# Optimization experiments

Measured on AMD Instinct MI355X. Metric: run time of the kernel, lower is better.

## Reference

```python
import jax, jax.numpy as jnp
import numpy as np
from jax import lax

EPS = 1e-5
QUANT_BITS = 16  # Conv2dShift default input fixed-point bits


def round_fixed(x, quant_bits=QUANT_BITS):
    # fixed-point rounding of activations with straight-through estimator
    scale = 2.0 ** (quant_bits - 1)
    xq = jnp.round(x * scale) / scale
    return x + lax.stop_gradient(xq - x)


def shift_conv3x3(x, w_shift, stride=1):
    # w_shift already holds sign * 2^shift power-of-two weights (see setup)
    x = round_fixed(x)
    return lax.conv_general_dilated(
        x, w_shift, window_strides=(stride, stride), padding=[(1, 1), (1, 1)],
        dimension_numbers=("NCHW", "OIHW", "NCHW"))


def adder_conv3x3(x, w):
    # AdderNet: out[n,co,h,w] = -sum_{ci,kh,kw} |patch - w[co,ci,kh,kw]|
    Co = w.shape[0]
    # patches: [N, C*3*3, H, W], feature ordering (c, kh, kw) matches w.reshape
    p = lax.conv_general_dilated_patches(
        x, filter_shape=(3, 3), window_strides=(1, 1), padding=[(1, 1), (1, 1)])
    wf = w.reshape(Co, -1)

    def per_out_channel(wc):  # wc: [C*9]
        return -jnp.sum(jnp.abs(p - wc[None, :, None, None]), axis=1)  # [N,H,W]

    out = lax.map(per_out_channel, wf)  # [Co, N, H, W] (sequential: bounds memory)
    return jnp.transpose(out, (1, 0, 2, 3))


def batch_norm(x, gamma, beta):
    # training-mode BN (batch statistics), matching nn.BatchNorm2d default forward
    m = jnp.mean(x, axis=(0, 2, 3), keepdims=True)
    v = jnp.var(x, axis=(0, 2, 3), keepdims=True)
    xn = (x - m) * lax.rsqrt(v + EPS)
    return xn * gamma.reshape(1, -1, 1, 1) + beta.reshape(1, -1, 1, 1)


def _quantize_shift_weights(w, weight_bits=5):
    # DeepShift PS: weight -> sign * 2^round(log2|w|), shift clipped
    sign = jnp.where(w >= 0, 1.0, -1.0)
    shift = jnp.round(jnp.log2(jnp.abs(w) + 1e-12))
    shift = jnp.clip(shift, -(2.0 ** (weight_bits - 1) - 1.0), 0.0)
    return sign * jnp.exp2(shift)


def setup_inputs() -> dict:
    key = jax.random.key(0)
    ks = jax.random.split(key, 9)
    N, C, H, W = 64, 128, 32, 32
    planes = 128
    fan = 1.0 / np.sqrt(C * 9)
    x = jax.random.normal(ks[0], (N, C, H, W), dtype=jnp.float32)
    w_shift1 = _quantize_shift_weights(
        jax.random.normal(ks[1], (planes, C, 3, 3), dtype=jnp.float32) * fan)
    w_add1 = jax.random.normal(ks[2], (planes, planes, 3, 3), dtype=jnp.float32) * fan
    w_shift2 = _quantize_shift_weights(
        jax.random.normal(ks[3], (planes, planes, 3, 3), dtype=jnp.float32) * fan)
    w_add2 = jax.random.normal(ks[4], (planes, planes, 3, 3), dtype=jnp.float32) * fan
    gamma1 = jnp.ones((planes,), jnp.float32)
    beta1 = jnp.zeros((planes,), jnp.float32)
    gamma2 = jnp.ones((planes,), jnp.float32)
    beta2 = jnp.zeros((planes,), jnp.float32)
    return {"x": x, "w_shift1": w_shift1, "w_add1": w_add1, "gamma1": gamma1,
            "beta1": beta1, "w_shift2": w_shift2, "w_add2": w_add2,
            "gamma2": gamma2, "beta2": beta2}


def reference(x, w_shift1, w_add1, gamma1, beta1, w_shift2, w_add2, gamma2, beta2):
    residual = x
    out = shift_conv3x3(x, w_shift1, stride=1)
    out = adder_conv3x3(out, w_add1)
    out = jax.nn.relu(batch_norm(out, gamma1, beta1))
    out = shift_conv3x3(out, w_shift2, stride=1)
    out = adder_conv3x3(out, w_add2)
    out = batch_norm(out, gamma2, beta2)
    out = jax.nn.relu(out + residual)
    return out
```

## Files before the change

### kernel.cpp

```cpp
#include <hip/hip_runtime.h>


#define NB   64
#define CIN  128
#define HW   32
#define COUT 128
constexpr int PLANE    = HW * HW;
constexpr int NPAIR    = CIN / 2;
constexpr int CI_CHUNK = 4;
constexpr int CO_CHUNK = 8;
constexpr int LPLANE   = 34 * 32;
constexpr int LDS_TOT  = 2 * CI_CHUNK * LPLANE;
constexpr int A_CI     = 2;
constexpr int A_CO     = 4;
constexpr int A_LDS    = 2 * A_CI * LPLANE;
constexpr float FSCALE    = 32768.0f;
constexpr float INV_SCALE = 1.0f / 32768.0f;
constexpr float QS     = 2048.0f;
constexpr float QB     = 32768.5f;
constexpr float INV_QS = 1.0f / 2048.0f;
constexpr unsigned PZ  = 0x80008000u;

constexpr int G_ROWB   = 32 * 8 * 16;
constexpr int G_CIQB   = 34 * G_ROWB;
constexpr int G_NB     = 4 * G_CIQB;

typedef _Float16 f16x8 __attribute__((ext_vector_type(8)));
typedef float    f32x4 __attribute__((ext_vector_type(4)));

#define GLOBAL_AS __attribute__((address_space(1)))
#define LDS_AS    __attribute__((address_space(3)))

__device__ __forceinline__ void gload_lds16(const void* g, void* l) {
    __builtin_amdgcn_global_load_lds((const GLOBAL_AS void*)g, (LDS_AS void*)l,
                                     16, 0, 0);
}
__device__ __forceinline__ float dpp_prev(float x) {
    return __int_as_float(__builtin_amdgcn_update_dpp(
        0, __float_as_int(x), 0x111, 0xF, 0xF, true));
}
__device__ __forceinline__ float dpp_next(float x) {
    return __int_as_float(__builtin_amdgcn_update_dpp(
        0, __float_as_int(x), 0x101, 0xF, 0xF, true));
}
__device__ __forceinline__ unsigned dpp_prev_u(unsigned x) {
    return (unsigned)__builtin_amdgcn_update_dpp(0, (int)x, 0x111, 0xF, 0xF, true);
}
__device__ __forceinline__ unsigned dpp_next_u(unsigned x) {
    return (unsigned)__builtin_amdgcn_update_dpp(0, (int)x, 0x101, 0xF, 0xF, true);
}
__device__ __forceinline__ uint4 dpp4_shr(uint4 v) {
    uint4 r;
    r.x = dpp_prev_u(v.x); r.y = dpp_prev_u(v.y);
    r.z = dpp_prev_u(v.z); r.w = dpp_prev_u(v.w);
    return r;
}
__device__ __forceinline__ uint4 dpp4_shl(uint4 v) {
    uint4 r;
    r.x = dpp_next_u(v.x); r.y = dpp_next_u(v.y);
    r.z = dpp_next_u(v.z); r.w = dpp_next_u(v.w);
    return r;
}
__device__ __forceinline__ void stage_plane4(const void* src, void* dst, int lane) {
#pragma unroll
    for (int i = 0; i < 4; ++i)
        gload_lds16((const char*)src + i * 1024 + lane * 16,
                    (char*)dst + 128 + i * 1024);
}
__device__ __forceinline__ unsigned q16(float a) {
    float t = fmaf(a, QS, QB);
    t = fminf(fmaxf(t, 0.0f), 65535.0f);
    return (unsigned)t;
}
__device__ __forceinline__ unsigned packhl(float v) {
    _Float16 h = (_Float16)v;
    _Float16 l = (_Float16)(v - (float)h);
    unsigned uh = (unsigned)__builtin_bit_cast(unsigned short, h);
    unsigned ul = (unsigned)__builtin_bit_cast(unsigned short, l);
    return uh | (ul << 16);
}

template <int WITH_BN>
__global__ __launch_bounds__(256) void transform_split(
    const float* __restrict__ in, const float* __restrict__ scale,
    const float* __restrict__ bias, uint4* __restrict__ G)
{
    __shared__ float sT[32 * 132];
    const int tid = threadIdx.x;
    const int b   = blockIdx.x;
    const int n   = b >> 5;
    const int ciq = (b >> 3) & 3;
    const int rq  = b & 7;

#pragma unroll
    for (int it = 0; it < 4; ++it) {
        int flat = it * 256 + tid;
        int ci_rel = flat >> 5;
        int px4 = (flat & 31) * 4;
        const float* ap = in + ((size_t)(n * CIN + ciq * 32 + ci_rel)) * PLANE
                             + rq * 128 + px4;
        float4 v = *reinterpret_cast<const float4*>(ap);
        if (WITH_BN) {
            float sc = scale[ciq * 32 + ci_rel], bs = bias[ciq * 32 + ci_rel];
            v.x = fmaxf(fmaf(v.x, sc, bs), 0.0f);
            v.y = fmaxf(fmaf(v.y, sc, bs), 0.0f);
            v.z = fmaxf(fmaf(v.z, sc, bs), 0.0f);
            v.w = fmaxf(fmaf(v.w, sc, bs), 0.0f);
        }
        v.x = rintf(v.x * FSCALE) * INV_SCALE;
        v.y = rintf(v.y * FSCALE) * INV_SCALE;
        v.z = rintf(v.z * FSCALE) * INV_SCALE;
        v.w = rintf(v.w * FSCALE) * INV_SCALE;
        *reinterpret_cast<float4*>(&sT[ci_rel * 132 + px4]) = v;
    }
    __syncthreads();

    uint4* Gp = G + ((size_t)n * G_NB + ciq * G_CIQB) / 16;
#pragma unroll
    for (int it = 0; it < 4; ++it) {
        int f = it * 256 + tid;
        int row_loc = f >> 8;
        int rem = f & 255;
        int w  = rem >> 3;
        int sg = rem & 7;
        int g  = sg ^ (w & 7);
        uint4 u;
        unsigned* up = &u.x;
#pragma unroll
        for (int j = 0; j < 4; ++j)
            up[j] = packhl(sT[(g * 4 + j) * 132 + row_loc * 32 + w]);
        int gr = rq * 4 + row_loc + 1;
        Gp[(gr * 32 + w) * 8 + sg] = u;
    }
    if (rq == 0) Gp[tid] = make_uint4(0, 0, 0, 0);
    if (rq == 7) Gp[33 * 256 + tid] = make_uint4(0, 0, 0, 0);
}

__global__ __launch_bounds__(256) void wf_prep(
    const float* __restrict__ w1, const float* __restrict__ w2,
    unsigned* __restrict__ WF)
{
    int i = blockIdx.x * 256 + threadIdx.x;
    int layer = i >= 147456;
    int idx = i - layer * 147456;
    int j2  = idx & 3;
    int l   = (idx >> 2) & 63;
    int cot = (idx >> 8) & 7;
    int kch = (idx >> 11) & 1;
    int ciq = (idx >> 12) & 3;
    int tap = idx >> 14;
    int ci  = ciq * 32 + kch * 16 + (l >> 4) * 4 + j2;
    int co  = cot * 16 + (l & 15);
    const float* w = layer ? w2 : w1;
    float v = w[((size_t)co * CIN + ci) * 9 + tap];
    unsigned h = (unsigned)__builtin_bit_cast(unsigned short, (_Float16)v);
    WF[i] = h | (h << 16);
}

__global__ __launch_bounds__(256, 2) void conv_mfma(
    const uint4* __restrict__ G, const uint4* __restrict__ WF,
    unsigned* __restrict__ P)
{
    __shared__ uint4 sA[1536];
    const int tid  = threadIdx.x;
    const int lane = tid & 63;
    const int wid  = tid >> 6;
    const int b    = (blockIdx.x & 7) * 64 + (blockIdx.x >> 3);
    const int n    = b >> 3;
    const int q4   = b & 7;
    const int glo16 = (lane >> 4) * 16;

    f32x4 acc[8][2];
#pragma unroll
    for (int i = 0; i < 8; ++i)
#pragma unroll
        for (int j = 0; j < 2; ++j) acc[i][j] = (f32x4){0.f, 0.f, 0.f, 0.f};

    for (int ciq = 0; ciq < 4; ++ciq) {
        if (ciq) __syncthreads();
        const char* src = (const char*)G + (size_t)n * G_NB + ciq * G_CIQB
                        + (size_t)q4 * 4 * G_ROWB;
#pragma unroll
        for (int i = 0; i < 6; ++i) {
            int off = i * 4096 + wid * 1024;
            gload_lds16(src + off + lane * 16, (char*)sA + off);
        }
        __syncthreads();

#pragma unroll
        for (int kch = 0; kch < 2; ++kch) {
            uint4 Brow[2][3];
            int pwh[2];
#pragma unroll
            for (int half = 0; half < 2; ++half) {
                pwh[half] = half * 16 + (lane & 15);
                int cb = ((kch * 64) | glo16) ^ ((pwh[half] & 7) * 16);
#pragma unroll
                for (int rr = 0; rr < 3; ++rr)
                    Brow[half][rr] = *reinterpret_cast<const uint4*>(
                        (const char*)sA + (wid + rr) * 4096 + pwh[half] * 128 + cb);
            }
#pragma unroll
            for (int dh = 0; dh < 3; ++dh)
#pragma unroll
            for (int dw = 0; dw < 3; ++dw) {
                const uint4* wfp = WF
                    + ((size_t)(((dh * 3 + dw) * 4 + ciq) * 2 + kch)) * 512 + lane;
                f16x8 a[8];
#pragma unroll
                for (int cot = 0; cot < 8; ++cot)
                    a[cot] = __builtin_bit_cast(f16x8, wfp[cot * 64]);
#pragma unroll
                for (int half = 0; half < 2; ++half) {
                    uint4 braw;
                    if (dw == 1) {
                        braw = Brow[half][dh];
                    } else if (dw == 0) {
                        if (half == 0) braw = dpp4_shr(Brow[0][dh]);
                        else {
                            int w2 = pwh[1] - 1;
                            braw = *reinterpret_cast<const uint4*>(
                                (const char*)sA + (wid + dh) * 4096 + w2 * 128
                                + (((kch * 64) | glo16) ^ ((w2 & 7) * 16)));
                        }
                    } else {
                        if (half == 1) braw = dpp4_shl(Brow[1][dh]);
                        else {
                            int w2 = pwh[0] + 1;
                            braw = *reinterpret_cast<const uint4*>(
                                (const char*)sA + (wid + dh) * 4096 + w2 * 128
                                + (((kch * 64) | glo16) ^ ((w2 & 7) * 16)));
                        }
                    }
                    f16x8 bf = __builtin_bit_cast(f16x8, braw);
#pragma unroll
                    for (int cot = 0; cot < 8; ++cot)
                        acc[cot][half] = __builtin_amdgcn_mfma_f32_16x16x32_f16(
                            a[cot], bf, acc[cot][half], 0, 0, 0);
                }
            }
        }
    }

    unsigned* Pn = P + (size_t)n * NPAIR * PLANE;
    const int r = q4 * 4 + wid;
#pragma unroll
    for (int cot = 0; cot < 8; ++cot) {
        int cp = cot * 8 + (lane >> 4) * 2;
#pragma unroll
        for (int p = 0; p < 2; ++p) {
            int px = r * 32 + p * 16 + (lane & 15);
            unsigned u01 = q16(acc[cot][p][0]) | (q16(acc[cot][p][1]) << 16);
            unsigned u23 = q16(acc[cot][p][2]) | (q16(acc[cot][p][3]) << 16);
            Pn[cp * PLANE + px] = u01;
            Pn[(cp + 1) * PLANE + px] = u23;
        }
    }
}

__global__ __launch_bounds__(256, 2) void conv_shift_valu(
    const float* __restrict__ in, const float* __restrict__ wgt,
    unsigned* __restrict__ out)
{
    __shared__ __align__(16) float sIn[LDS_TOT];
    const int tid  = threadIdx.x;
    const int lane = tid & 63;
    const int wid  = tid >> 6;
    const int bid  = (blockIdx.x & 7) * 128 + (blockIdx.x >> 3);
    const int n    = bid >> 4;
    const int co0  = (bid & 15) * CO_CHUNK;
    const int r    = tid >> 3;
    const int c    = tid & 7;
    const int c0   = c * 4;
    const bool cz  = (c == 0), c7 = (c == 7);

    float acc[4][CO_CHUNK];
#pragma unroll
    for (int p = 0; p < 4; ++p)
#pragma unroll
        for (int co = 0; co < CO_CHUNK; ++co) acc[p][co] = 0.0f;

    const float* inN = in + (size_t)n * CIN * PLANE;
    for (int idx = tid; idx < 512; idx += 256) {
        int slot = idx >> 6, wq = idx & 63;
        sIn[slot * LPLANE + (wq < 32 ? wq : 1024 + wq)] = 0.0f;
    }
    stage_plane4(inN + wid * PLANE, sIn + wid * LPLANE, lane);
    __syncthreads();

    int cur = 0;
    for (int ci0 = 0; ci0 < CIN; ci0 += CI_CHUNK) {
        if (ci0 + CI_CHUNK < CIN)
            stage_plane4(inN + (size_t)(ci0 + CI_CHUNK + wid) * PLANE,
                         sIn + ((cur ^ 1) * CI_CHUNK + wid) * LPLANE, lane);
        const float* sb = sIn + cur * CI_CHUNK * LPLANE;
#pragma unroll
        for (int cc = 0; cc < CI_CHUNK; ++cc) {
            float w[3][6];
#pragma unroll
            for (int dh = 0; dh < 3; ++dh) {
                const float* sp = sb + cc * LPLANE + (r + dh) * 32 + c0;
                float4 qv = *reinterpret_cast<const float4*>(sp);
                qv.x = rintf(qv.x * FSCALE) * INV_SCALE;
                qv.y = rintf(qv.y * FSCALE) * INV_SCALE;
                qv.z = rintf(qv.z * FSCALE) * INV_SCALE;
                qv.w = rintf(qv.w * FSCALE) * INV_SCALE;
                float lf = dpp_prev(qv.w);
                float rt = dpp_next(qv.x);
                w[dh][0] = cz ? 0.0f : lf;
                w[dh][1] = qv.x; w[dh][2] = qv.y; w[dh][3] = qv.z; w[dh][4] = qv.w;
                w[dh][5] = c7 ? 0.0f : rt;
            }
            const float* wp = wgt + ((size_t)co0 * CIN + (ci0 + cc)) * 9;
#pragma unroll
            for (int co = 0; co < CO_CHUNK; ++co)
#pragma unroll
                for (int dh = 0; dh < 3; ++dh)
#pragma unroll
                    for (int dw = 0; dw < 3; ++dw) {
                        const float wvv = wp[(size_t)co * CIN * 9 + dh * 3 + dw];
#pragma unroll
                        for (int p = 0; p < 4; ++p)
                            acc[p][co] = fmaf(w[dh][p + dw], wvv, acc[p][co]);
                    }
        }
        __syncthreads();
        cur ^= 1;
    }
    unsigned* outP = out + ((size_t)n * NPAIR + co0 / 2) * PLANE + r * HW + c0;
#pragma unroll
    for (int pr = 0; pr < CO_CHUNK / 2; ++pr) {
        uint4 v;
        unsigned* vp = &v.x;
#pragma unroll
        for (int p = 0; p < 4; ++p)
            vp[p] = q16(acc[p][2 * pr]) | (q16(acc[p][2 * pr + 1]) << 16);
        *reinterpret_cast<uint4*>(&outP[pr * PLANE]) = v;
    }
}

__global__ __launch_bounds__(256) void bn_relu_inplace(
    float4* __restrict__ io, const float* __restrict__ scale,
    const float* __restrict__ bias)
{
    int i = blockIdx.x * 256 + threadIdx.x;
    int c = (i >> 8) & 127;
    float sc = scale[c], bs = bias[c];
    float4 v = io[i];
    v.x = fmaxf(fmaf(v.x, sc, bs), 0.0f);
    v.y = fmaxf(fmaf(v.y, sc, bs), 0.0f);
    v.z = fmaxf(fmaf(v.z, sc, bs), 0.0f);
    v.w = fmaxf(fmaf(v.w, sc, bs), 0.0f);
    io[i] = v;
}

__global__ __launch_bounds__(256, 8) void adder_packed(
    const unsigned* __restrict__ in, const unsigned* __restrict__ wq,
    float* __restrict__ out, double* __restrict__ ssum, double* __restrict__ ssq)
{
    __shared__ __align__(16) unsigned sIn[A_LDS];
    const int tid  = threadIdx.x;
    const int lane = tid & 63;
    const int wid  = tid >> 6;
    const int bid  = (blockIdx.x & 7) * 256 + (blockIdx.x >> 3);
    const int n    = bid >> 5;
    const int co0  = (bid & 31) * A_CO;
    const int r    = tid >> 3;
    const int c    = tid & 7;
    const int c0   = c * 4;
    const bool cz  = (c == 0), c7 = (c == 7);
    const unsigned pz = PZ;

    unsigned acc[4][A_CO];
#pragma unroll
    for (int p = 0; p < 4; ++p)
#pragma unroll
        for (int co = 0; co < A_CO; ++co) acc[p][co] = 0u;

    const unsigned* inN = in + (size_t)n * NPAIR * PLANE;
    {
        int slot = tid >> 6, wqi = tid & 63;
        sIn[slot * LPLANE + (wqi < 32 ? wqi : 1024 + wqi)] = PZ;
    }
    if (wid < A_CI)
        stage_plane4(inN + wid * PLANE, sIn + wid * LPLANE, lane);
    __syncthreads();

    int cur = 0;
    for (int s = 0; s < NPAIR / A_CI; ++s) {
        if (s + 1 < NPAIR / A_CI && wid < A_CI)
            stage_plane4(inN + (size_t)((s + 1) * A_CI + wid) * PLANE,
                         sIn + ((cur ^ 1) * A_CI + wid) * LPLANE, lane);
        const unsigned* sb = sIn + cur * A_CI * LPLANE;
#pragma unroll
        for (int cc = 0; cc < A_CI; ++cc) {
            unsigned wi[3][6];
#pragma unroll
            for (int dh = 0; dh < 3; ++dh) {
                const unsigned* sp = sb + cc * LPLANE + (r + dh) * 32 + c0;
                uint4 qv = *reinterpret_cast<const uint4*>(sp);
                unsigned lf = dpp_prev_u(qv.w);
                unsigned rt = dpp_next_u(qv.x);
                wi[dh][0] = cz ? pz : lf;
                wi[dh][1] = qv.x; wi[dh][2] = qv.y; wi[dh][3] = qv.z; wi[dh][4] = qv.w;
                wi[dh][5] = c7 ? pz : rt;
            }
            const int cp = s * A_CI + cc;
            const unsigned* wrow = wq + ((size_t)co0 * NPAIR + cp) * 9;
#pragma unroll
            for (int co = 0; co < A_CO; ++co)
#pragma unroll
                for (int dh = 0; dh < 3; ++dh)
#pragma unroll
                    for (int dw = 0; dw < 3; ++dw) {
                        const unsigned wv =
                            wrow[(size_t)co * NPAIR * 9 + dh * 3 + dw];
#pragma unroll
                        for (int p = 0; p < 4; ++p)
                            asm("v_sad_u16 %0, %1, %2, %0"
                                : "+v"(acc[p][co])
                                : "v"(wi[dh][p + dw]), "s"(wv));
                    }
        }
        __syncthreads();
        cur ^= 1;
    }

    float* outP = out + ((size_t)n * COUT + co0) * PLANE + r * HW + c0;
#pragma unroll
    for (int co = 0; co < A_CO; ++co) {
        float y0 = -(float)acc[0][co] * INV_QS;
        float y1 = -(float)acc[1][co] * INV_QS;
        float y2 = -(float)acc[2][co] * INV_QS;
        float y3 = -(float)acc[3][co] * INV_QS;
        *reinterpret_cast<float4*>(&outP[co * PLANE]) = make_float4(y0, y1, y2, y3);
        float s = (y0 + y1) + (y2 + y3);
        float q = fmaf(y0, y0, y1 * y1) + fmaf(y2, y2, y3 * y3);
#pragma unroll
        for (int m = 32; m > 0; m >>= 1) {
            s += __shfl_xor(s, m, 64);
            q += __shfl_xor(q, m, 64);
        }
        if (lane == 0) {
            atomicAdd(&ssum[co0 + co], (double)s);
            atomicAdd(&ssq [co0 + co], (double)q);
        }
    }
}

__global__ __launch_bounds__(256) void quant_pack_weights(
    const float* __restrict__ w1, const float* __restrict__ w2,
    unsigned* __restrict__ wq)
{
    int i = blockIdx.x * 256 + threadIdx.x;
    int layer = i >= 73728;
    int j   = i - layer * 73728;
    int co  = j / 576;
    int rem = j - co * 576;
    int cp  = rem / 9;
    int tap = rem - cp * 9;
    const float* w = layer ? w2 : w1;
    float f0 = w[((size_t)co * CIN + 2 * cp) * 9 + tap];
    float f1 = w[((size_t)co * CIN + 2 * cp + 1) * 9 + tap];
    wq[i] = q16(f0) | (q16(f1) << 16);
}

__global__ void zero_stats(double* st) {
    int i = threadIdx.x;
    st[i] = 0.0; st[i + 256] = 0.0;
}

__global__ void finalize_bn(const double* __restrict__ ssum, const double* __restrict__ ssq,
                            const float* __restrict__ gamma, const float* __restrict__ beta,
                            float* __restrict__ scale, float* __restrict__ bias)
{
    int c = threadIdx.x;
    const double cnt = (double)NB * PLANE;
    double m   = ssum[c] / cnt;
    double var = ssq[c] / cnt - m * m;
    double rstd = 1.0 / sqrt(var + 1e-5);
    float sc = (float)((double)gamma[c] * rstd);
    scale[c] = sc;
    bias[c]  = beta[c] - (float)m * sc;
}

__global__ __launch_bounds__(256) void bn_add_relu(
    float4* __restrict__ io, const float4* __restrict__ res,
    const float* __restrict__ scale, const float* __restrict__ bias)
{
    int i = blockIdx.x * 256 + threadIdx.x;
    int c = (i >> 8) & 127;
    float sc = scale[c], bs = bias[c];
    float4 v = io[i];
    float4 x = res[i];
    v.x = fmaxf(fmaf(v.x, sc, bs) + x.x, 0.0f);
    v.y = fmaxf(fmaf(v.y, sc, bs) + x.y, 0.0f);
    v.z = fmaxf(fmaf(v.z, sc, bs) + x.z, 0.0f);
    v.w = fmaxf(fmaf(v.w, sc, bs) + x.w, 0.0f);
    io[i] = v;
}

extern "C" void kernel_launch(void* const* d_in, const int* in_sizes, int n_in,
                              void* d_out, int out_size, void* d_ws, size_t ws_size,
                              hipStream_t stream)
{
    const float* x    = (const float*)d_in[0];
    const float* wS1  = (const float*)d_in[1];
    const float* wA1  = (const float*)d_in[2];
    const float* g1   = (const float*)d_in[3];
    const float* b1   = (const float*)d_in[4];
    const float* wS2  = (const float*)d_in[5];
    const float* wA2  = (const float*)d_in[6];
    const float* g2   = (const float*)d_in[7];
    const float* b2   = (const float*)d_in[8];
    float* outp = (float*)d_out;

    char* ws = (char*)d_ws;
    const size_t MFMA_WS = 54204416;
    const bool mf = ws_size >= MFMA_WS;

    unsigned* P = (unsigned*)ws;
    double* st; float* sb; unsigned* wq; char* Gb = nullptr; unsigned* WF = nullptr;
    if (mf) {
        Gb = ws + 16777216;
        st = (double*)(ws + 52428800);
        sb = (float*)(ws + 52432896);
        wq = (unsigned*)(ws + 52434944);
        WF = (unsigned*)(ws + 53024768);
    } else {
        st = (double*)(ws + 16777216);
        sb = (float*)(st + 512);
        wq = (unsigned*)(sb + 512);
    }
    double* s1 = st,       *q1 = st + 128;
    double* s2 = st + 256, *q2 = st + 384;
    float* sc1 = sb,       *bi1 = sb + 128;
    float* sc2 = sb + 256, *bi2 = sb + 384;

    const int adderGrid = NB * (COUT / A_CO);
    const int ewGrid    = (NB * COUT * PLANE / 4) / 256;

    zero_stats<<<1, 256, 0, stream>>>(st);
    quant_pack_weights<<<576, 256, 0, stream>>>(wA1, wA2, wq);

    if (mf) {
        wf_prep<<<1152, 256, 0, stream>>>(wS1, wS2, WF);
        transform_split<0><<<2048, 256, 0, stream>>>(x, nullptr, nullptr, (uint4*)Gb);
        conv_mfma<<<512, 256, 0, stream>>>((const uint4*)Gb, (const uint4*)WF, P);
        adder_packed<<<adderGrid, 256, 0, stream>>>(P, wq, outp, s1, q1);
        finalize_bn<<<1, 128, 0, stream>>>(s1, q1, g1, b1, sc1, bi1);
        transform_split<1><<<2048, 256, 0, stream>>>(outp, sc1, bi1, (uint4*)Gb);
        conv_mfma<<<512, 256, 0, stream>>>((const uint4*)Gb,
                                           (const uint4*)(WF + 147456), P);
        adder_packed<<<adderGrid, 256, 0, stream>>>(P, wq + 73728, outp, s2, q2);
        finalize_bn<<<1, 128, 0, stream>>>(s2, q2, g2, b2, sc2, bi2);
        bn_add_relu<<<ewGrid, 256, 0, stream>>>((float4*)outp, (const float4*)x,
                                                sc2, bi2);
    } else {
        conv_shift_valu<<<1024, 256, 0, stream>>>(x, wS1, P);
        adder_packed<<<adderGrid, 256, 0, stream>>>(P, wq, outp, s1, q1);
        finalize_bn<<<1, 128, 0, stream>>>(s1, q1, g1, b1, sc1, bi1);
        bn_relu_inplace<<<ewGrid, 256, 0, stream>>>((float4*)outp, sc1, bi1);
        conv_shift_valu<<<1024, 256, 0, stream>>>(outp, wS2, P);
        adder_packed<<<adderGrid, 256, 0, stream>>>(P, wq + 73728, outp, s2, q2);
        finalize_bn<<<1, 128, 0, stream>>>(s2, q2, g2, b2, sc2, bi2);
        bn_add_relu<<<ewGrid, 256, 0, stream>>>((float4*)outp, (const float4*)x,
                                                sc2, bi2);
    }
}
```

Measured before the change: 465.1 us.

## Give each adder wave private LDS row slabs and drop block barriers

Each wave in the adder kernel now stages its own 8-row slab plus halo rows of two channel-pair planes into a private LDS region with async global-to-LDS loads. Double buffering is controlled by per-wave waitcnt instead of a block-wide __syncthreads, so waves no longer stall on one another and all four waves share the loading. The stats zeroing is folded into the weight-quantize kernel, which removes one launch. The cost is redundant halo-row loads and reliance on precise vmcnt/lgkmcnt ordering for correctness.

```diff
diff --git a/kernel.cpp b/kernel.cpp
--- a/kernel.cpp
+++ b/kernel.cpp
@@ -11,9 +11,7 @@
 constexpr int CO_CHUNK = 8;
 constexpr int LPLANE   = 34 * 32;
 constexpr int LDS_TOT  = 2 * CI_CHUNK * LPLANE;
-constexpr int A_CI     = 2;
 constexpr int A_CO     = 4;
-constexpr int A_LDS    = 2 * A_CI * LPLANE;
 constexpr float FSCALE    = 32768.0f;
 constexpr float INV_SCALE = 1.0f / 32768.0f;
 constexpr float QS     = 2048.0f;
@@ -358,7 +356,7 @@
     const unsigned* __restrict__ in, const unsigned* __restrict__ wq,
     float* __restrict__ out, double* __restrict__ ssum, double* __restrict__ ssq)
 {
-    __shared__ __align__(16) unsigned sIn[A_LDS];
+    __shared__ __align__(16) unsigned sIn[5120];
     const int tid  = threadIdx.x;
     const int lane = tid & 63;
     const int wid  = tid >> 6;
@@ -371,6 +369,23 @@
     const bool cz  = (c == 0), c7 = (c == 7);
     const unsigned pz = PZ;
 
+    unsigned* sW  = sIn + wid * 1280;
+    const int r0    = wid * 8;
+    const int gRow0 = (wid == 0) ? 0 : (r0 - 1);
+    const int slot0 = (wid == 0) ? 1 : 0;
+    const int nrows = (wid == 0 || wid == 3) ? 9 : 10;
+    const int rem   = nrows * 128 - 1024;
+
+    if (wid == 0 || wid == 3) {
+        const int so = (wid == 0) ? 0 : 9 * 32;
+#pragma unroll
+        for (int k = 0; k < 2; ++k) {
+            int f = k * 64 + lane;
+            int b = f >> 6, p = (f >> 5) & 1, col = f & 31;
+            sW[b * 640 + p * 320 + so + col] = pz;
+        }
+    }
+
     unsigned acc[4][A_CO];
 #pragma unroll
     for (int p = 0; p < 4; ++p)
@@ -378,26 +393,40 @@
         for (int co = 0; co < A_CO; ++co) acc[p][co] = 0u;
 
     const unsigned* inN = in + (size_t)n * NPAIR * PLANE;
-    {
-        int slot = tid >> 6, wqi = tid & 63;
-        sIn[slot * LPLANE + (wqi < 32 ? wqi : 1024 + wqi)] = PZ;
-    }
-    if (wid < A_CI)
-        stage_plane4(inN + wid * PLANE, sIn + wid * LPLANE, lane);
-    __syncthreads();
-
-    int cur = 0;
-    for (int s = 0; s < NPAIR / A_CI; ++s) {
-        if (s + 1 < NPAIR / A_CI && wid < A_CI)
-            stage_plane4(inN + (size_t)((s + 1) * A_CI + wid) * PLANE,
-                         sIn + ((cur ^ 1) * A_CI + wid) * LPLANE, lane);
-        const unsigned* sb = sIn + cur * A_CI * LPLANE;
-#pragma unroll
-        for (int cc = 0; cc < A_CI; ++cc) {
+
+    auto stage2 = [&](int cpBase, int buf) {
+#pragma unroll
+        for (int pl = 0; pl < 2; ++pl) {
+            const char* gsrc = (const char*)(inN + (size_t)(cpBase + pl) * PLANE
+                                             + gRow0 * 32);
+            char* ldst = (char*)(sW + buf * 640 + pl * 320 + slot0 * 32);
+            gload_lds16(gsrc + lane * 16, ldst);
+            if (lane * 16 < rem)
+                gload_lds16(gsrc + 1024 + lane * 16, ldst + 1024);
+        }
+    };
+
+    stage2(0, 0);
+
+    for (int s = 0; s < NPAIR / 2; ++s) {
+        const int buf = s & 1;
+        if (s + 1 < NPAIR / 2) {
+            asm volatile("s_waitcnt lgkmcnt(0)" ::: "memory");
+            stage2(2 * (s + 1), buf ^ 1);
+            asm volatile("s_waitcnt vmcnt(4)" ::: "memory");
+        } else {
+            asm volatile("s_waitcnt vmcnt(0)" ::: "memory");
+        }
+        __builtin_amdgcn_sched_barrier(0);
+
+        const unsigned* sb = sW + buf * 640;
+#pragma unroll
+        for (int cc = 0; cc < 2; ++cc) {
             unsigned wi[3][6];
 #pragma unroll
             for (int dh = 0; dh < 3; ++dh) {
-                const unsigned* sp = sb + cc * LPLANE + (r + dh) * 32 + c0;
+                const unsigned* sp = sb + cc * 320
+                                   + ((lane >> 3) + dh) * 32 + c0;
                 uint4 qv = *reinterpret_cast<const uint4*>(sp);
                 unsigned lf = dpp_prev_u(qv.w);
                 unsigned rt = dpp_next_u(qv.x);
@@ -405,7 +434,7 @@
                 wi[dh][1] = qv.x; wi[dh][2] = qv.y; wi[dh][3] = qv.z; wi[dh][4] = qv.w;
                 wi[dh][5] = c7 ? pz : rt;
             }
-            const int cp = s * A_CI + cc;
+            const int cp = 2 * s + cc;
             const unsigned* wrow = wq + ((size_t)co0 * NPAIR + cp) * 9;
 #pragma unroll
             for (int co = 0; co < A_CO; ++co)
@@ -422,8 +451,6 @@
                                 : "v"(wi[dh][p + dw]), "s"(wv));
                     }
         }
-        __syncthreads();
-        cur ^= 1;
     }
 
     float* outP = out + ((size_t)n * COUT + co0) * PLANE + r * HW + c0;
@@ -450,9 +477,12 @@
 
 __global__ __launch_bounds__(256) void quant_pack_weights(
     const float* __restrict__ w1, const float* __restrict__ w2,
-    unsigned* __restrict__ wq)
+    unsigned* __restrict__ wqo, double* __restrict__ st)
 {
     int i = blockIdx.x * 256 + threadIdx.x;
+    if (blockIdx.x == 0) {
+        st[threadIdx.x] = 0.0; st[threadIdx.x + 256] = 0.0;
+    }
     int layer = i >= 73728;
     int j   = i - layer * 73728;
     int co  = j / 576;
@@ -462,12 +492,7 @@
     const float* w = layer ? w2 : w1;
     float f0 = w[((size_t)co * CIN + 2 * cp) * 9 + tap];
     float f1 = w[((size_t)co * CIN + 2 * cp + 1) * 9 + tap];
-    wq[i] = q16(f0) | (q16(f1) << 16);
-}
-
-__global__ void zero_stats(double* st) {
-    int i = threadIdx.x;
-    st[i] = 0.0; st[i + 256] = 0.0;
+    wqo[i] = q16(f0) | (q16(f1) << 16);
 }
 
 __global__ void finalize_bn(const double* __restrict__ ssum, const double* __restrict__ ssq,
@@ -540,8 +565,7 @@
     const int adderGrid = NB * (COUT / A_CO);
     const int ewGrid    = (NB * COUT * PLANE / 4) / 256;
 
-    zero_stats<<<1, 256, 0, stream>>>(st);
-    quant_pack_weights<<<576, 256, 0, stream>>>(wA1, wA2, wq);
+    quant_pack_weights<<<576, 256, 0, stream>>>(wA1, wA2, wq, st);
 
     if (mf) {
         wf_prep<<<1152, 256, 0, stream>>>(wS1, wS2, WF);
```

New measurement: 469.4 us. About the same (+0.9%).

## Read adder inputs directly from global memory instead of LDS double-buffering

Applied to the files above, without the earlier changes.

The adder kernel no longer stages input channel-pair planes into shared memory with a double buffer and barriers. Each thread now loads its three needed rows straight from global memory (relying on L1/L2 caching), substituting padding values at the top and bottom borders. It also folds the stats-zeroing kernel into the weight-quantization kernel to save one launch. This removes the LDS traffic and __syncthreads but makes every channel iteration depend on global-load latency and re-reads each row three times through the cache.

```diff
diff --git a/kernel.cpp b/kernel.cpp
--- a/kernel.cpp
+++ b/kernel.cpp
@@ -11,9 +11,7 @@
 constexpr int CO_CHUNK = 8;
 constexpr int LPLANE   = 34 * 32;
 constexpr int LDS_TOT  = 2 * CI_CHUNK * LPLANE;
-constexpr int A_CI     = 2;
 constexpr int A_CO     = 4;
-constexpr int A_LDS    = 2 * A_CI * LPLANE;
 constexpr float FSCALE    = 32768.0f;
 constexpr float INV_SCALE = 1.0f / 32768.0f;
 constexpr float QS     = 2048.0f;
@@ -354,14 +352,12 @@
     io[i] = v;
 }
 
-__global__ __launch_bounds__(256, 8) void adder_packed(
+__global__ __launch_bounds__(256, 8) void adder_direct(
     const unsigned* __restrict__ in, const unsigned* __restrict__ wq,
     float* __restrict__ out, double* __restrict__ ssum, double* __restrict__ ssq)
 {
-    __shared__ __align__(16) unsigned sIn[A_LDS];
     const int tid  = threadIdx.x;
     const int lane = tid & 63;
-    const int wid  = tid >> 6;
     const int bid  = (blockIdx.x & 7) * 256 + (blockIdx.x >> 3);
     const int n    = bid >> 5;
     const int co0  = (bid & 31) * A_CO;
@@ -369,61 +365,57 @@
     const int c    = tid & 7;
     const int c0   = c * 4;
     const bool cz  = (c == 0), c7 = (c == 7);
+    const bool rz  = (r == 0), r31 = (r == 31);
     const unsigned pz = PZ;
 
+    const char* base = (const char*)(in + (size_t)n * NPAIR * PLANE);
+    const int off_lo  = (rz  ? 0  : (r - 1)) * 128 + c0 * 4;
+    const int off_mid = r * 128 + c0 * 4;
+    const int off_hi  = (r31 ? 31 : (r + 1)) * 128 + c0 * 4;
+
     unsigned acc[4][A_CO];
 #pragma unroll
     for (int p = 0; p < 4; ++p)
 #pragma unroll
         for (int co = 0; co < A_CO; ++co) acc[p][co] = 0u;
 
-    const unsigned* inN = in + (size_t)n * NPAIR * PLANE;
-    {
-        int slot = tid >> 6, wqi = tid & 63;
-        sIn[slot * LPLANE + (wqi < 32 ? wqi : 1024 + wqi)] = PZ;
-    }
-    if (wid < A_CI)
-        stage_plane4(inN + wid * PLANE, sIn + wid * LPLANE, lane);
-    __syncthreads();
-
-    int cur = 0;
-    for (int s = 0; s < NPAIR / A_CI; ++s) {
-        if (s + 1 < NPAIR / A_CI && wid < A_CI)
-            stage_plane4(inN + (size_t)((s + 1) * A_CI + wid) * PLANE,
-                         sIn + ((cur ^ 1) * A_CI + wid) * LPLANE, lane);
-        const unsigned* sb = sIn + cur * A_CI * LPLANE;
-#pragma unroll
-        for (int cc = 0; cc < A_CI; ++cc) {
-            unsigned wi[3][6];
-#pragma unroll
-            for (int dh = 0; dh < 3; ++dh) {
-                const unsigned* sp = sb + cc * LPLANE + (r + dh) * 32 + c0;
-                uint4 qv = *reinterpret_cast<const uint4*>(sp);
-                unsigned lf = dpp_prev_u(qv.w);
-                unsigned rt = dpp_next_u(qv.x);
-                wi[dh][0] = cz ? pz : lf;
-                wi[dh][1] = qv.x; wi[dh][2] = qv.y; wi[dh][3] = qv.z; wi[dh][4] = qv.w;
-                wi[dh][5] = c7 ? pz : rt;
-            }
-            const int cp = s * A_CI + cc;
-            const unsigned* wrow = wq + ((size_t)co0 * NPAIR + cp) * 9;
-#pragma unroll
-            for (int co = 0; co < A_CO; ++co)
-#pragma unroll
-                for (int dh = 0; dh < 3; ++dh)
-#pragma unroll
-                    for (int dw = 0; dw < 3; ++dw) {
-                        const unsigned wv =
-                            wrow[(size_t)co * NPAIR * 9 + dh * 3 + dw];
-#pragma unroll
-                        for (int p = 0; p < 4; ++p)
-                            asm("v_sad_u16 %0, %1, %2, %0"
-                                : "+v"(acc[p][co])
-                                : "v"(wi[dh][p + dw]), "s"(wv));
-                    }
-        }
-        __syncthreads();
-        cur ^= 1;
+#pragma unroll 2
+    for (int cp = 0; cp < NPAIR; ++cp) {
+        const char* pb = base + cp * 4096;
+        uint4 qrow[3];
+        qrow[0] = *reinterpret_cast<const uint4*>(pb + off_lo);
+        qrow[1] = *reinterpret_cast<const uint4*>(pb + off_mid);
+        qrow[2] = *reinterpret_cast<const uint4*>(pb + off_hi);
+        qrow[0].x = rz ? pz : qrow[0].x;  qrow[0].y = rz ? pz : qrow[0].y;
+        qrow[0].z = rz ? pz : qrow[0].z;  qrow[0].w = rz ? pz : qrow[0].w;
+        qrow[2].x = r31 ? pz : qrow[2].x; qrow[2].y = r31 ? pz : qrow[2].y;
+        qrow[2].z = r31 ? pz : qrow[2].z; qrow[2].w = r31 ? pz : qrow[2].w;
+
+        unsigned wi[3][6];
+#pragma unroll
+        for (int dh = 0; dh < 3; ++dh) {
+            uint4 qv = qrow[dh];
+            unsigned lf = dpp_prev_u(qv.w);
+            unsigned rt = dpp_next_u(qv.x);
+            wi[dh][0] = cz ? pz : lf;
+            wi[dh][1] = qv.x; wi[dh][2] = qv.y; wi[dh][3] = qv.z; wi[dh][4] = qv.w;
+            wi[dh][5] = c7 ? pz : rt;
+        }
+
+        const unsigned* wrow = wq + ((size_t)co0 * NPAIR + cp) * 9;
+#pragma unroll
+        for (int co = 0; co < A_CO; ++co)
+#pragma unroll
+            for (int dh = 0; dh < 3; ++dh)
+#pragma unroll
+                for (int dw = 0; dw < 3; ++dw) {
+                    const unsigned wv = wrow[(size_t)co * NPAIR * 9 + dh * 3 + dw];
+#pragma unroll
+                    for (int p = 0; p < 4; ++p)
+                        asm("v_sad_u16 %0, %1, %2, %0"
+                            : "+v"(acc[p][co])
+                            : "v"(wi[dh][p + dw]), "s"(wv));
+                }
     }
 
     float* outP = out + ((size_t)n * COUT + co0) * PLANE + r * HW + c0;
@@ -450,9 +442,12 @@
 
 __global__ __launch_bounds__(256) void quant_pack_weights(
     const float* __restrict__ w1, const float* __restrict__ w2,
-    unsigned* __restrict__ wq)
+    unsigned* __restrict__ wqo, double* __restrict__ st)
 {
     int i = blockIdx.x * 256 + threadIdx.x;
+    if (blockIdx.x == 0) {
+        st[threadIdx.x] = 0.0; st[threadIdx.x + 256] = 0.0;
+    }
     int layer = i >= 73728;
     int j   = i - layer * 73728;
     int co  = j / 576;
@@ -462,12 +457,7 @@
     const float* w = layer ? w2 : w1;
     float f0 = w[((size_t)co * CIN + 2 * cp) * 9 + tap];
     float f1 = w[((size_t)co * CIN + 2 * cp + 1) * 9 + tap];
-    wq[i] = q16(f0) | (q16(f1) << 16);
-}
-
-__global__ void zero_stats(double* st) {
-    int i = threadIdx.x;
-    st[i] = 0.0; st[i + 256] = 0.0;
+    wqo[i] = q16(f0) | (q16(f1) << 16);
 }
 
 __global__ void finalize_bn(const double* __restrict__ ssum, const double* __restrict__ ssq,
@@ -540,29 +530,28 @@
     const int adderGrid = NB * (COUT / A_CO);
     const int ewGrid    = (NB * COUT * PLANE / 4) / 256;
 
-    zero_stats<<<1, 256, 0, stream>>>(st);
-    quant_pack_weights<<<576, 256, 0, stream>>>(wA1, wA2, wq);
+    quant_pack_weights<<<576, 256, 0, stream>>>(wA1, wA2, wq, st);
 
     if (mf) {
         wf_prep<<<1152, 256, 0, stream>>>(wS1, wS2, WF);
         transform_split<0><<<2048, 256, 0, stream>>>(x, nullptr, nullptr, (uint4*)Gb);
         conv_mfma<<<512, 256, 0, stream>>>((const uint4*)Gb, (const uint4*)WF, P);
-        adder_packed<<<adderGrid, 256, 0, stream>>>(P, wq, outp, s1, q1);
+        adder_direct<<<adderGrid, 256, 0, stream>>>(P, wq, outp, s1, q1);
         finalize_bn<<<1, 128, 0, stream>>>(s1, q1, g1, b1, sc1, bi1);
         transform_split<1><<<2048, 256, 0, stream>>>(outp, sc1, bi1, (uint4*)Gb);
         conv_mfma<<<512, 256, 0, stream>>>((const uint4*)Gb,
                                            (const uint4*)(WF + 147456), P);
-        adder_packed<<<adderGrid, 256, 0, stream>>>(P, wq + 73728, outp, s2, q2);
+        adder_direct<<<adderGrid, 256, 0, stream>>>(P, wq + 73728, outp, s2, q2);
         finalize_bn<<<1, 128, 0, stream>>>(s2, q2, g2, b2, sc2, bi2);
         bn_add_relu<<<ewGrid, 256, 0, stream>>>((float4*)outp, (const float4*)x,
                                                 sc2, bi2);
     } else {
         conv_shift_valu<<<1024, 256, 0, stream>>>(x, wS1, P);
-        adder_packed<<<adderGrid, 256, 0, stream>>>(P, wq, outp, s1, q1);
+        adder_direct<<<adderGrid, 256, 0, stream>>>(P, wq, outp, s1, q1);
         finalize_bn<<<1, 128, 0, stream>>>(s1, q1, g1, b1, sc1, bi1);
         bn_relu_inplace<<<ewGrid, 256, 0, stream>>>((float4*)outp, sc1, bi1);
         conv_shift_valu<<<1024, 256, 0, stream>>>(outp, wS2, P);
-        adder_packed<<<adderGrid, 256, 0, stream>>>(P, wq + 73728, outp, s2, q2);
+        adder_direct<<<adderGrid, 256, 0, stream>>>(P, wq + 73728, outp, s2, q2);
         finalize_bn<<<1, 128, 0, stream>>>(s2, q2, g2, b2, sc2, bi2);
         bn_add_relu<<<ewGrid, 256, 0, stream>>>((float4*)outp, (const float4*)x,
                                                 sc2, bi2);
```

Result: slower. 491.1 us (+5.6%).

## Drop hi/lo fp16 split in shift conv, double-buffer staging, merge prep kernels

Applied to the files above, without the earlier changes.

The activation transform now stores a single fp16 value per element instead of a hi+lo fp16 pair. This halves the G buffer and removes the second K-chunk of MFMA work in conv_mfma. conv_mfma gains per-wave double-buffered LDS staging with vmcnt waits in place of block-wide syncs, and the adder kernel stages all four planes up front. The weight quantization, weight prep and stats-zeroing kernels are fused into one launch. Dropping the low fp16 part risks accuracy, since 16-bit fixed-point activations are not exactly representable in fp16.

```diff
diff --git a/kernel.cpp b/kernel.cpp
--- a/kernel.cpp
+++ b/kernel.cpp
@@ -11,9 +11,7 @@
 constexpr int CO_CHUNK = 8;
 constexpr int LPLANE   = 34 * 32;
 constexpr int LDS_TOT  = 2 * CI_CHUNK * LPLANE;
-constexpr int A_CI     = 2;
 constexpr int A_CO     = 4;
-constexpr int A_LDS    = 2 * A_CI * LPLANE;
 constexpr float FSCALE    = 32768.0f;
 constexpr float INV_SCALE = 1.0f / 32768.0f;
 constexpr float QS     = 2048.0f;
@@ -21,7 +19,7 @@
 constexpr float INV_QS = 1.0f / 2048.0f;
 constexpr unsigned PZ  = 0x80008000u;
 
-constexpr int G_ROWB   = 32 * 8 * 16;
+constexpr int G_ROWB   = 32 * 4 * 16;
 constexpr int G_CIQB   = 34 * G_ROWB;
 constexpr int G_NB     = 4 * G_CIQB;
 
@@ -30,6 +28,8 @@
 
 #define GLOBAL_AS __attribute__((address_space(1)))
 #define LDS_AS    __attribute__((address_space(3)))
+
+__device__ __forceinline__ int fsw(int w) { return (w & 3) ^ ((w >> 2) & 3); }
 
 __device__ __forceinline__ void gload_lds16(const void* g, void* l) {
     __builtin_amdgcn_global_load_lds((const GLOBAL_AS void*)g, (LDS_AS void*)l,
@@ -72,12 +72,8 @@
     t = fminf(fmaxf(t, 0.0f), 65535.0f);
     return (unsigned)t;
 }
-__device__ __forceinline__ unsigned packhl(float v) {
-    _Float16 h = (_Float16)v;
-    _Float16 l = (_Float16)(v - (float)h);
-    unsigned uh = (unsigned)__builtin_bit_cast(unsigned short, h);
-    unsigned ul = (unsigned)__builtin_bit_cast(unsigned short, l);
-    return uh | (ul << 16);
+__device__ __forceinline__ unsigned short f16b(float v) {
+    return __builtin_bit_cast(unsigned short, (_Float16)v);
 }
 
 template <int WITH_BN>
@@ -117,58 +113,83 @@
 
     uint4* Gp = G + ((size_t)n * G_NB + ciq * G_CIQB) / 16;
 #pragma unroll
-    for (int it = 0; it < 4; ++it) {
+    for (int it = 0; it < 2; ++it) {
         int f = it * 256 + tid;
-        int row_loc = f >> 8;
-        int rem = f & 255;
-        int w  = rem >> 3;
-        int sg = rem & 7;
-        int g  = sg ^ (w & 7);
+        int row_loc = f >> 7;
+        int rem = f & 127;
+        int w  = rem >> 2;
+        int sg = rem & 3;
+        int g  = sg ^ fsw(w);
         uint4 u;
         unsigned* up = &u.x;
 #pragma unroll
-        for (int j = 0; j < 4; ++j)
-            up[j] = packhl(sT[(g * 4 + j) * 132 + row_loc * 32 + w]);
+        for (int j2 = 0; j2 < 4; ++j2) {
+            unsigned lo = f16b(sT[(g * 8 + 2 * j2)     * 132 + row_loc * 32 + w]);
+            unsigned hi = f16b(sT[(g * 8 + 2 * j2 + 1) * 132 + row_loc * 32 + w]);
+            up[j2] = lo | (hi << 16);
+        }
         int gr = rq * 4 + row_loc + 1;
-        Gp[(gr * 32 + w) * 8 + sg] = u;
-    }
-    if (rq == 0) Gp[tid] = make_uint4(0, 0, 0, 0);
-    if (rq == 7) Gp[33 * 256 + tid] = make_uint4(0, 0, 0, 0);
-}
-
-__global__ __launch_bounds__(256) void wf_prep(
-    const float* __restrict__ w1, const float* __restrict__ w2,
-    unsigned* __restrict__ WF)
+        Gp[(gr * 32 + w) * 4 + sg] = u;
+    }
+    if (rq == 0 && tid < 128) Gp[tid] = make_uint4(0, 0, 0, 0);
+    if (rq == 7 && tid < 128) Gp[33 * 128 + tid] = make_uint4(0, 0, 0, 0);
+}
+
+__global__ __launch_bounds__(256) void prep_weights(
+    const float* __restrict__ a1, const float* __restrict__ a2,
+    const float* __restrict__ s1w, const float* __restrict__ s2w,
+    unsigned* __restrict__ wqo, unsigned* __restrict__ WFd,
+    double* __restrict__ st)
 {
     int i = blockIdx.x * 256 + threadIdx.x;
-    int layer = i >= 147456;
-    int idx = i - layer * 147456;
-    int j2  = idx & 3;
-    int l   = (idx >> 2) & 63;
-    int cot = (idx >> 8) & 7;
-    int kch = (idx >> 11) & 1;
-    int ciq = (idx >> 12) & 3;
-    int tap = idx >> 14;
-    int ci  = ciq * 32 + kch * 16 + (l >> 4) * 4 + j2;
-    int co  = cot * 16 + (l & 15);
-    const float* w = layer ? w2 : w1;
-    float v = w[((size_t)co * CIN + ci) * 9 + tap];
-    unsigned h = (unsigned)__builtin_bit_cast(unsigned short, (_Float16)v);
-    WF[i] = h | (h << 16);
+    if (blockIdx.x == 0) {
+        st[threadIdx.x] = 0.0; st[threadIdx.x + 256] = 0.0;
+    }
+    if (i < 147456) {
+        int layer = i >= 73728;
+        int j   = i - layer * 73728;
+        int co  = j / 576;
+        int rem = j - co * 576;
+        int cp  = rem / 9;
+        int tap = rem - cp * 9;
+        const float* w = layer ? a2 : a1;
+        float f0 = w[((size_t)co * CIN + 2 * cp) * 9 + tap];
+        float f1 = w[((size_t)co * CIN + 2 * cp + 1) * 9 + tap];
+        wqo[i] = q16(f0) | (q16(f1) << 16);
+    } else {
+        int j = i - 147456;
+        int layer = j >= 73728;
+        int idx = j - layer * 73728;
+        int j2  = idx & 3;
+        int l   = (idx >> 2) & 63;
+        int cot = (idx >> 8) & 7;
+        int ciq = (idx >> 11) & 3;
+        int tap = idx >> 13;
+        int ci  = ciq * 32 + (l >> 4) * 8 + j2 * 2;
+        int co  = cot * 16 + (l & 15);
+        const float* w = layer ? s2w : s1w;
+        unsigned lo = f16b(w[((size_t)co * CIN + ci) * 9 + tap]);
+        unsigned hi = f16b(w[((size_t)co * CIN + ci + 1) * 9 + tap]);
+        WFd[layer * 73728 + idx] = lo | (hi << 16);
+    }
 }
 
 __global__ __launch_bounds__(256, 2) void conv_mfma(
     const uint4* __restrict__ G, const uint4* __restrict__ WF,
     unsigned* __restrict__ P)
 {
-    __shared__ uint4 sA[1536];
+    __shared__ uint4 sA[3072];
     const int tid  = threadIdx.x;
     const int lane = tid & 63;
     const int wid  = tid >> 6;
     const int b    = (blockIdx.x & 7) * 64 + (blockIdx.x >> 3);
     const int n    = b >> 3;
     const int q4   = b & 7;
-    const int glo16 = (lane >> 4) * 16;
+    const int gsg  = lane >> 4;
+
+    char* myL = (char*)sA + wid * 12288;
+    const char* src = (const char*)G + (size_t)n * G_NB + (size_t)q4 * 4 * G_ROWB
+                    + wid * 2048;
 
     f32x4 acc[8][2];
 #pragma unroll
@@ -176,68 +197,74 @@
 #pragma unroll
         for (int j = 0; j < 2; ++j) acc[i][j] = (f32x4){0.f, 0.f, 0.f, 0.f};
 
+    auto stage = [&](int ciq, int buf) {
+        const char* s = src + ciq * G_CIQB;
+#pragma unroll
+        for (int rr = 0; rr < 3; ++rr)
+#pragma unroll
+            for (int k = 0; k < 2; ++k)
+                gload_lds16(s + rr * 2048 + k * 1024 + lane * 16,
+                            myL + buf * 6144 + rr * 2048 + k * 1024);
+    };
+
+    stage(0, 0);
     for (int ciq = 0; ciq < 4; ++ciq) {
-        if (ciq) __syncthreads();
-        const char* src = (const char*)G + (size_t)n * G_NB + ciq * G_CIQB
-                        + (size_t)q4 * 4 * G_ROWB;
-#pragma unroll
-        for (int i = 0; i < 6; ++i) {
-            int off = i * 4096 + wid * 1024;
-            gload_lds16(src + off + lane * 16, (char*)sA + off);
-        }
-        __syncthreads();
-
-#pragma unroll
-        for (int kch = 0; kch < 2; ++kch) {
-            uint4 Brow[2][3];
-            int pwh[2];
+        const int buf = ciq & 1;
+        if (ciq < 3) {
+            stage(ciq + 1, buf ^ 1);
+            asm volatile("s_waitcnt vmcnt(6)" ::: "memory");
+        } else {
+            asm volatile("s_waitcnt vmcnt(0)" ::: "memory");
+        }
+        __builtin_amdgcn_sched_barrier(0);
+
+        uint4 Brow[2][3];
+        int pwh[2];
+#pragma unroll
+        for (int half = 0; half < 2; ++half) {
+            pwh[half] = half * 16 + (lane & 15);
+#pragma unroll
+            for (int rr = 0; rr < 3; ++rr)
+                Brow[half][rr] = *reinterpret_cast<const uint4*>(
+                    myL + buf * 6144 + rr * 2048 + pwh[half] * 64
+                    + ((gsg ^ fsw(pwh[half])) * 16));
+        }
+#pragma unroll
+        for (int dh = 0; dh < 3; ++dh)
+#pragma unroll
+        for (int dw = 0; dw < 3; ++dw) {
+            const uint4* wfp = WF + ((size_t)((dh * 3 + dw) * 4 + ciq)) * 512 + lane;
+            f16x8 a[8];
+#pragma unroll
+            for (int cot = 0; cot < 8; ++cot)
+                a[cot] = __builtin_bit_cast(f16x8, wfp[cot * 64]);
 #pragma unroll
             for (int half = 0; half < 2; ++half) {
-                pwh[half] = half * 16 + (lane & 15);
-                int cb = ((kch * 64) | glo16) ^ ((pwh[half] & 7) * 16);
-#pragma unroll
-                for (int rr = 0; rr < 3; ++rr)
-                    Brow[half][rr] = *reinterpret_cast<const uint4*>(
-                        (const char*)sA + (wid + rr) * 4096 + pwh[half] * 128 + cb);
-            }
-#pragma unroll
-            for (int dh = 0; dh < 3; ++dh)
-#pragma unroll
-            for (int dw = 0; dw < 3; ++dw) {
-                const uint4* wfp = WF
-                    + ((size_t)(((dh * 3 + dw) * 4 + ciq) * 2 + kch)) * 512 + lane;
-                f16x8 a[8];
+                uint4 braw;
+                if (dw == 1) {
+                    braw = Brow[half][dh];
+                } else if (dw == 0) {
+                    if (half == 0) braw = dpp4_shr(Brow[0][dh]);
+                    else {
+                        int w2 = pwh[1] - 1;
+                        braw = *reinterpret_cast<const uint4*>(
+                            myL + buf * 6144 + dh * 2048 + w2 * 64
+                            + ((gsg ^ fsw(w2)) * 16));
+                    }
+                } else {
+                    if (half == 1) braw = dpp4_shl(Brow[1][dh]);
+                    else {
+                        int w2 = pwh[0] + 1;
+                        braw = *reinterpret_cast<const uint4*>(
+                            myL + buf * 6144 + dh * 2048 + w2 * 64
+                            + ((gsg ^ fsw(w2)) * 16));
+                    }
+                }
+                f16x8 bf = __builtin_bit_cast(f16x8, braw);
 #pragma unroll
                 for (int cot = 0; cot < 8; ++cot)
-                    a[cot] = __builtin_bit_cast(f16x8, wfp[cot * 64]);
-#pragma unroll
-                for (int half = 0; half < 2; ++half) {
-                    uint4 braw;
-                    if (dw == 1) {
-                        braw = Brow[half][dh];
-                    } else if (dw == 0) {
-                        if (half == 0) braw = dpp4_shr(Brow[0][dh]);
-                        else {
-                            int w2 = pwh[1] - 1;
-                            braw = *reinterpret_cast<const uint4*>(
-                                (const char*)sA + (wid + dh) * 4096 + w2 * 128
-                                + (((kch * 64) | glo16) ^ ((w2 & 7) * 16)));
-                        }
-                    } else {
-                        if (half == 1) braw = dpp4_shl(Brow[1][dh]);
-                        else {
-                            int w2 = pwh[0] + 1;
-                            braw = *reinterpret_cast<const uint4*>(
-                                (const char*)sA + (wid + dh) * 4096 + w2 * 128
-                                + (((kch * 64) | glo16) ^ ((w2 & 7) * 16)));
-                        }
-                    }
-                    f16x8 bf = __builtin_bit_cast(f16x8, braw);
-#pragma unroll
-                    for (int cot = 0; cot < 8; ++cot)
-                        acc[cot][half] = __builtin_amdgcn_mfma_f32_16x16x32_f16(
-                            a[cot], bf, acc[cot][half], 0, 0, 0);
-                }
+                    acc[cot][half] = __builtin_amdgcn_mfma_f32_16x16x32_f16(
+                        a[cot], bf, acc[cot][half], 0, 0, 0);
             }
         }
     }
@@ -358,7 +385,7 @@
     const unsigned* __restrict__ in, const unsigned* __restrict__ wq,
     float* __restrict__ out, double* __restrict__ ssum, double* __restrict__ ssq)
 {
-    __shared__ __align__(16) unsigned sIn[A_LDS];
+    __shared__ __align__(16) unsigned sIn[4 * LPLANE];
     const int tid  = threadIdx.x;
     const int lane = tid & 63;
     const int wid  = tid >> 6;
@@ -371,29 +398,31 @@
     const bool cz  = (c == 0), c7 = (c == 7);
     const unsigned pz = PZ;
 
-    unsigned acc[4][A_CO];
-#pragma unroll
-    for (int p = 0; p < 4; ++p)
-#pragma unroll
-        for (int co = 0; co < A_CO; ++co) acc[p][co] = 0u;
-
-    const unsigned* inN = in + (size_t)n * NPAIR * PLANE;
     {
         int slot = tid >> 6, wqi = tid & 63;
-        sIn[slot * LPLANE + (wqi < 32 ? wqi : 1024 + wqi)] = PZ;
-    }
-    if (wid < A_CI)
-        stage_plane4(inN + wid * PLANE, sIn + wid * LPLANE, lane);
+        sIn[slot * LPLANE + (wqi < 32 ? wqi : 1024 + wqi)] = pz;
+    }
+
+    unsigned acc[4][A_CO];
+#pragma unroll
+    for (int p = 0; p < 4; ++p)
+#pragma unroll
+        for (int co = 0; co < A_CO; ++co) acc[p][co] = 0u;
+
+    const unsigned* inN = in + (size_t)n * NPAIR * PLANE;
+
+    stage_plane4(inN + (size_t)wid * PLANE, sIn + wid * LPLANE, lane);
     __syncthreads();
 
     int cur = 0;
-    for (int s = 0; s < NPAIR / A_CI; ++s) {
-        if (s + 1 < NPAIR / A_CI && wid < A_CI)
-            stage_plane4(inN + (size_t)((s + 1) * A_CI + wid) * PLANE,
-                         sIn + ((cur ^ 1) * A_CI + wid) * LPLANE, lane);
-        const unsigned* sb = sIn + cur * A_CI * LPLANE;
-#pragma unroll
-        for (int cc = 0; cc < A_CI; ++cc) {
+    for (int s = 0; s < NPAIR / 2; ++s) {
+        if (s >= 1 && s + 1 < NPAIR / 2 && wid < 2)
+            stage_plane4(inN + (size_t)(2 * (s + 1) + wid) * PLANE,
+                         sIn + ((cur ^ 1) * 2 + wid) * LPLANE, lane);
+
+        const unsigned* sb = sIn + cur * 2 * LPLANE;
+#pragma unroll
+        for (int cc = 0; cc < 2; ++cc) {
             unsigned wi[3][6];
 #pragma unroll
             for (int dh = 0; dh < 3; ++dh) {
@@ -405,7 +434,7 @@
                 wi[dh][1] = qv.x; wi[dh][2] = qv.y; wi[dh][3] = qv.z; wi[dh][4] = qv.w;
                 wi[dh][5] = c7 ? pz : rt;
             }
-            const int cp = s * A_CI + cc;
+            const int cp = 2 * s + cc;
             const unsigned* wrow = wq + ((size_t)co0 * NPAIR + cp) * 9;
 #pragma unroll
             for (int co = 0; co < A_CO; ++co)
@@ -446,28 +475,6 @@
             atomicAdd(&ssq [co0 + co], (double)q);
         }
     }
-}
-
-__global__ __launch_bounds__(256) void quant_pack_weights(
-    const float* __restrict__ w1, const float* __restrict__ w2,
-    unsigned* __restrict__ wq)
-{
-    int i = blockIdx.x * 256 + threadIdx.x;
-    int layer = i >= 73728;
-    int j   = i - layer * 73728;
-    int co  = j / 576;
-    int rem = j - co * 576;
-    int cp  = rem / 9;
-    int tap = rem - cp * 9;
-    const float* w = layer ? w2 : w1;
-    float f0 = w[((size_t)co * CIN + 2 * cp) * 9 + tap];
-    float f1 = w[((size_t)co * CIN + 2 * cp + 1) * 9 + tap];
-    wq[i] = q16(f0) | (q16(f1) << 16);
-}
-
-__global__ void zero_stats(double* st) {
-    int i = threadIdx.x;
-    st[i] = 0.0; st[i + 256] = 0.0;
 }
 
 __global__ void finalize_bn(const double* __restrict__ ssum, const double* __restrict__ ssq,
@@ -516,17 +523,17 @@
     float* outp = (float*)d_out;
 
     char* ws = (char*)d_ws;
-    const size_t MFMA_WS = 54204416;
+    const size_t MFMA_WS = 35788800;
     const bool mf = ws_size >= MFMA_WS;
 
     unsigned* P = (unsigned*)ws;
     double* st; float* sb; unsigned* wq; char* Gb = nullptr; unsigned* WF = nullptr;
     if (mf) {
         Gb = ws + 16777216;
-        st = (double*)(ws + 52428800);
-        sb = (float*)(ws + 52432896);
-        wq = (unsigned*)(ws + 52434944);
-        WF = (unsigned*)(ws + 53024768);
+        st = (double*)(ws + 34603008);
+        sb = (float*)(ws + 34607104);
+        wq = (unsigned*)(ws + 34609152);
+        WF = (unsigned*)(ws + 35198976);
     } else {
         st = (double*)(ws + 16777216);
         sb = (float*)(st + 512);
@@ -540,23 +547,22 @@
     const int adderGrid = NB * (COUT / A_CO);
     const int ewGrid    = (NB * COUT * PLANE / 4) / 256;
 
-    zero_stats<<<1, 256, 0, stream>>>(st);
-    quant_pack_weights<<<576, 256, 0, stream>>>(wA1, wA2, wq);
-
     if (mf) {
-        wf_prep<<<1152, 256, 0, stream>>>(wS1, wS2, WF);
+        prep_weights<<<1152, 256, 0, stream>>>(wA1, wA2, wS1, wS2, wq, WF, st);
         transform_split<0><<<2048, 256, 0, stream>>>(x, nullptr, nullptr, (uint4*)Gb);
         conv_mfma<<<512, 256, 0, stream>>>((const uint4*)Gb, (const uint4*)WF, P);
         adder_packed<<<adderGrid, 256, 0, stream>>>(P, wq, outp, s1, q1);
         finalize_bn<<<1, 128, 0, stream>>>(s1, q1, g1, b1, sc1, bi1);
         transform_split<1><<<2048, 256, 0, stream>>>(outp, sc1, bi1, (uint4*)Gb);
         conv_mfma<<<512, 256, 0, stream>>>((const uint4*)Gb,
-                                           (const uint4*)(WF + 147456), P);
+                                           (const uint4*)WF + 18432, P);
         adder_packed<<<adderGrid, 256, 0, stream>>>(P, wq + 73728, outp, s2, q2);
         finalize_bn<<<1, 128, 0, stream>>>(s2, q2, g2, b2, sc2, bi2);
         bn_add_relu<<<ewGrid, 256, 0, stream>>>((float4*)outp, (const float4*)x,
                                                 sc2, bi2);
     } else {
+        prep_weights<<<1152, 256, 0, stream>>>(wA1, wA2, wS1, wS2, wq,
+                                               (unsigned*)ws, st);
         conv_shift_valu<<<1024, 256, 0, stream>>>(x, wS1, P);
         adder_packed<<<adderGrid, 256, 0, stream>>>(P, wq, outp, s1, q1);
         finalize_bn<<<1, 128, 0, stream>>>(s1, q1, g1, b1, sc1, bi1);
```

New measurement: 420.7 us. 1.11x faster.
